# Kernel optimization log

Hardware: AMD Instinct MI355X
Metric: run time of the kernel (lower is better)

## Reference

```python
import jax, jax.numpy as jnp
import numpy as np

B, C, N, K = 2, 64, 16384, 16
C_OUT = 64


def setup_inputs() -> dict:
    key = jax.random.key(0)
    k1, k2, k3, k4 = jax.random.split(key, 4)
    x = jax.random.normal(k1, (B, C, N), dtype=jnp.float32)
    edge_index = jax.random.randint(k2, (2, B, N, K), 0, N, dtype=jnp.int64)
    # 1x1 Conv2d params: weight [C_out, 3C], bias [C_out]
    W = jax.random.normal(k3, (C_OUT, 3 * C), dtype=jnp.float32) * (1.0 / np.sqrt(3 * C))
    b = jax.random.normal(k4, (C_OUT,), dtype=jnp.float32) * 0.01
    return {"x": x, "edge_index": edge_index, "W": W, "b": b}


def _gather_nodes(x, idx):
    # x: [B, C, N], idx: [B, N, K] -> [B, C, N, K]
    return jax.vmap(lambda xb, ib: xb[:, ib])(x, idx)


def reference(x, edge_index, W, b):
    # x: [B, C, N]; edge_index: [2, B, N, K]
    x_i = _gather_nodes(x, edge_index[1])          # center features  [B,C,N,K]
    x_j = _gather_nodes(x, edge_index[0])          # neighbor features [B,C,N,K]
    edge_features = x_j - x_i                      # [B,C,N,K]
    global_feature = jnp.mean(x, axis=2, keepdims=True)  # [B,C,1] global mean over nodes
    global_rep = jnp.broadcast_to(global_feature[..., None], x_i.shape)  # [B,C,N,K]
    combined = jnp.concatenate([x_i, edge_features, global_rep], axis=1)  # [B,3C,N,K]
    # BasicConv: 1x1 conv + ReLU (norm=None)
    out = jnp.einsum("bcnk,oc->bonk", combined, W) + b[None, :, None, None]
    out = jax.nn.relu(out)
    return jnp.max(out, axis=-1, keepdims=True)    # [B,C_out,N,1]
```

## Files before the change

kernel.cpp:

```cpp
#include <hip/hip_runtime.h>


#define NNODES 16384
#define NCH 64

typedef _Float16 half8 __attribute__((ext_vector_type(8)));
typedef float f32x2 __attribute__((ext_vector_type(2)));
typedef float f32x4 __attribute__((ext_vector_type(4)));

__global__ __launch_bounds__(64) void prep_kernel(const float* __restrict__ W,
                                                  float2* __restrict__ ABg,
                                                  float* __restrict__ g_slots) {
  int o = blockIdx.x;
  int t = threadIdx.x;
  if (o == 0) {
#pragma unroll
    for (int i = 0; i < 16; ++i) g_slots[t + i * 64] = 0.0f;
  }
  float w1 = W[o * 192 + t];
  float w2 = W[o * 192 + 64 + t];
  ABg[t * 64 + o] = make_float2(w1 - w2, w2);
}

__global__ __launch_bounds__(256) void warmx_kernel(const float* __restrict__ x) {
  int t = threadIdx.x;
  int blk = blockIdx.x;
  int b = blk >> 8;
  int mb = (blk & 255) * 64;
  const float* xb = x + (size_t)b * (NCH * NNODES) + mb;
  int off = t & 15;
  float keep = 0.f;
#pragma unroll
  for (int j = 0; j < 4; ++j) {
    int c = (t >> 4) + j * 16;
    f32x4 q = *(const f32x4*)(xb + (size_t)c * NNODES + off * 4);
    keep += q.x;
  }
  asm volatile("" ::"v"(keep));
}

__global__ __launch_bounds__(256) void uv_kernel(const float* __restrict__ x,
                                                 const float2* __restrict__ ABg,
                                                 _Float16* __restrict__ u,
                                                 _Float16* __restrict__ v,
                                                 float* __restrict__ g_slots) {
  __shared__ float2 ABs[64 * 64];
  __shared__ float xs[64][64];
  __shared__ float csumS[64];
  int t = threadIdx.x;
  int lane = t & 63;
  int wv = __builtin_amdgcn_readfirstlane(t >> 6);
  int blk = blockIdx.x;
  int b = blk >> 8;
  int mb = (blk & 255) * 64;

  const float* xb = x + (size_t)b * (NCH * NNODES) + mb;
  int off = t & 15;
  f32x4 q0, q1, q2, q3;
  {
    q0 = __builtin_nontemporal_load((const f32x4*)(xb + (size_t)((t >> 4) + 0) * NNODES + off * 4));
    q1 = __builtin_nontemporal_load((const f32x4*)(xb + (size_t)((t >> 4) + 16) * NNODES + off * 4));
    q2 = __builtin_nontemporal_load((const f32x4*)(xb + (size_t)((t >> 4) + 32) * NNODES + off * 4));
    q3 = __builtin_nontemporal_load((const f32x4*)(xb + (size_t)((t >> 4) + 48) * NNODES + off * 4));
  }
  {
    const float4* src = (const float4*)ABg;
    float4* dst = (float4*)ABs;
#pragma unroll
    for (int j = 0; j < 8; ++j) dst[t + j * 256] = src[t + j * 256];
  }
  {
    f32x4 qq[4] = {q0, q1, q2, q3};
#pragma unroll
    for (int j = 0; j < 4; ++j) {
      int c = (t >> 4) + j * 16;
      *(f32x4*)&xs[c][off * 4] = qq[j];
      float s = (qq[j].x + qq[j].y) + (qq[j].z + qq[j].w);
      s += __shfl_xor(s, 1, 16);
      s += __shfl_xor(s, 2, 16);
      s += __shfl_xor(s, 4, 16);
      s += __shfl_xor(s, 8, 16);
      if (off == 0) csumS[c] = s;
    }
  }
  __syncthreads();
  if (t < 64) atomicAdd(&g_slots[((blk & 7) << 7) + b * 64 + t], csumS[t]);

  int m0 = wv * 16;
  f32x2 aU[8], aV[8];
#pragma unroll
  for (int i = 0; i < 8; ++i) {
    aU[i] = (f32x2){0.f, 0.f};
    aV[i] = (f32x2){0.f, 0.f};
  }
#pragma unroll 8
  for (int c = 0; c < 64; ++c) {
    float2 ab = ABs[c * 64 + lane];
    f32x2 a2 = {ab.x, ab.x};
    f32x2 b2 = {ab.y, ab.y};
    const f32x4* xr = (const f32x4*)&xs[c][m0];
    f32x4 p0q = xr[0];
    f32x4 p1q = xr[1];
    f32x4 p2q = xr[2];
    f32x4 p3q = xr[3];
    f32x2 p0 = {p0q.x, p0q.y}, p1 = {p0q.z, p0q.w};
    f32x2 p2 = {p1q.x, p1q.y}, p3 = {p1q.z, p1q.w};
    f32x2 p4 = {p2q.x, p2q.y}, p5 = {p2q.z, p2q.w};
    f32x2 p6 = {p3q.x, p3q.y}, p7 = {p3q.z, p3q.w};
    aU[0] = __builtin_elementwise_fma(a2, p0, aU[0]);
    aU[1] = __builtin_elementwise_fma(a2, p1, aU[1]);
    aU[2] = __builtin_elementwise_fma(a2, p2, aU[2]);
    aU[3] = __builtin_elementwise_fma(a2, p3, aU[3]);
    aU[4] = __builtin_elementwise_fma(a2, p4, aU[4]);
    aU[5] = __builtin_elementwise_fma(a2, p5, aU[5]);
    aU[6] = __builtin_elementwise_fma(a2, p6, aU[6]);
    aU[7] = __builtin_elementwise_fma(a2, p7, aU[7]);
    aV[0] = __builtin_elementwise_fma(b2, p0, aV[0]);
    aV[1] = __builtin_elementwise_fma(b2, p1, aV[1]);
    aV[2] = __builtin_elementwise_fma(b2, p2, aV[2]);
    aV[3] = __builtin_elementwise_fma(b2, p3, aV[3]);
    aV[4] = __builtin_elementwise_fma(b2, p4, aV[4]);
    aV[5] = __builtin_elementwise_fma(b2, p5, aV[5]);
    aV[6] = __builtin_elementwise_fma(b2, p6, aV[6]);
    aV[7] = __builtin_elementwise_fma(b2, p7, aV[7]);
  }
  _Float16* ub = u + ((size_t)b * NNODES + mb + m0) * NCH + lane;
  _Float16* vb = v + ((size_t)b * NNODES + mb + m0) * NCH + lane;
#pragma unroll
  for (int i = 0; i < 8; ++i) {
    __builtin_nontemporal_store((_Float16)aU[i][0], &ub[(2 * i) * NCH]);
    __builtin_nontemporal_store((_Float16)aU[i][1], &ub[(2 * i + 1) * NCH]);
    __builtin_nontemporal_store((_Float16)aV[i][0], &vb[(2 * i) * NCH]);
    __builtin_nontemporal_store((_Float16)aV[i][1], &vb[(2 * i + 1) * NCH]);
  }
}

__global__ __launch_bounds__(256) void gather_kernel(const int* __restrict__ ei,
                                                     const _Float16* __restrict__ u,
                                                     const _Float16* __restrict__ v,
                                                     const float* __restrict__ W,
                                                     const float* __restrict__ bias,
                                                     const float* __restrict__ g_slots,
                                                     float* __restrict__ out) {
  __shared__ float tile[64][33];
  __shared__ float gb[64];
  __shared__ float pg[4][64];
  __shared__ float G_s[64];
  int t = threadIdx.x;
  int lane = t & 63;
  int wv = t >> 6;
  int blk = blockIdx.x;
  int xcd = blk & 7;
  int b = xcd >> 2;
  int nb = (blk >> 3) * 4 + (xcd & 3);
  int n0 = nb * 32;
  int q = lane >> 3;
  int r = lane & 7;
  const int* e0b = ei + (size_t)b * NNODES * 16;
  const int* e1b = ei + (size_t)(2 + b) * NNODES * 16;
  int f0 = (n0 + wv * 8) * 16 + q * 16 + r;
  int i0a = __builtin_nontemporal_load(e0b + f0);
  int i0b = __builtin_nontemporal_load(e0b + f0 + 8);
  int i1a = __builtin_nontemporal_load(e1b + f0);
  int i1b = __builtin_nontemporal_load(e1b + f0 + 8);
  if (t < 64) {
    float s = 0.f;
#pragma unroll
    for (int sl = 0; sl < 8; ++sl) s += g_slots[sl * 128 + b * 64 + t];
    gb[t] = s * (1.0f / 16384.0f);
  }
  __syncthreads();
  {
    int o = t >> 2, cq = t & 3;
    const float4* wr = (const float4*)(W + o * 192 + 128 + cq * 16);
    const float4* gr = (const float4*)(gb + cq * 16);
    float s = 0.f;
#pragma unroll
    for (int j = 0; j < 4; ++j) {
      float4 w = wr[j];
      float4 gg = gr[j];
      s += w.x * gg.x + w.y * gg.y + w.z * gg.z + w.w * gg.w;
    }
    pg[cq][o] = s;
  }
  __syncthreads();
  if (t < 64) G_s[t] = bias[t] + ((pg[0][t] + pg[1][t]) + (pg[2][t] + pg[3][t]));
  __syncthreads();
  const char* ubase = (const char*)(u + (size_t)b * NNODES * NCH);
  const char* vbase = (const char*)(v + (size_t)b * NNODES * NCH);
  uint32_t r16 = (uint32_t)(r * 16);
  half8 accA, accB;
#pragma unroll
  for (int j = 0; j < 8; ++j) {
    accA[j] = (_Float16)(-60000.0f);
    accB[j] = (_Float16)(-60000.0f);
  }
#pragma unroll
  for (int h = 0; h < 2; ++h) {
    half8 ua[8], va[8];
#pragma unroll
    for (int k = 0; k < 8; ++k) {
      int src = (lane & 56) + k;
      int m1 = __shfl(h ? i1b : i1a, src, 64);
      int m0i = __shfl(h ? i0b : i0a, src, 64);
      ua[k] = *(const half8*)(ubase + ((uint32_t)m1 * 128u + r16));
      va[k] = *(const half8*)(vbase + ((uint32_t)m0i * 128u + r16));
    }
#pragma unroll
    for (int k = 0; k < 8; ++k) {
      half8 s = ua[k] + va[k];
      if (k & 1)
        accB = __builtin_elementwise_max(accB, s);
      else
        accA = __builtin_elementwise_max(accA, s);
    }
  }
  half8 acc = __builtin_elementwise_max(accA, accB);
  int col = wv * 8 + q;
#pragma unroll
  for (int j = 0; j < 8; ++j) {
    tile[r * 8 + j][col] = fmaxf((float)acc[j] + G_s[r * 8 + j], 0.0f);
  }
  __syncthreads();
#pragma unroll
  for (int j = 0; j < 8; ++j) {
    int o = (t >> 5) + j * 8;
    int c2 = t & 31;
    __builtin_nontemporal_store(tile[o][c2],
                                &out[((size_t)b * 64 + o) * NNODES + n0 + c2]);
  }
}

extern "C" void kernel_launch(void* const* d_in, const int* in_sizes, int n_in,
                              void* d_out, int out_size, void* d_ws, size_t ws_size,
                              hipStream_t stream) {
  const float* x = (const float*)d_in[0];
  const int* ei = (const int*)d_in[1];
  const float* W = (const float*)d_in[2];
  const float* bias = (const float*)d_in[3];
  float* out = (float*)d_out;

  char* ws = (char*)d_ws;
  _Float16* u = (_Float16*)ws;
  _Float16* v = (_Float16*)(ws + (size_t)4 * 1024 * 1024);
  float* g_slots = (float*)(ws + (size_t)8 * 1024 * 1024);
  float2* ABg = (float2*)(ws + (size_t)8 * 1024 * 1024 + 4096);

  prep_kernel<<<64, 64, 0, stream>>>(W, ABg, g_slots);
  warmx_kernel<<<512, 256, 0, stream>>>(x);
  uv_kernel<<<512, 256, 0, stream>>>(x, ABg, u, v, g_slots);
  gather_kernel<<<1024, 256, 0, stream>>>(ei, u, v, W, bias, g_slots, out);
}
```

Before: 90.83 us.

## Fold weight prep into uv kernel, prefetch edge indices, drop nontemporal loads

Removes the separate prep kernel: each uv block builds its shared weight table directly from W, and the global-sum slots are zeroed with hipMemsetAsync. The warm-up kernel now streams through both x and the edge-index array, and the later nontemporal loads become ordinary loads. The intent is to pull those inputs into cache before the main kernels read them and to cut one launch. In exchange, every uv block re-reads and transposes W with strided loads, and the warm pass adds extra memory traffic of its own.

```diff
diff --git a/kernel.cpp b/kernel.cpp
--- a/kernel.cpp
+++ b/kernel.cpp
@@ -8,39 +8,21 @@
 typedef float f32x2 __attribute__((ext_vector_type(2)));
 typedef float f32x4 __attribute__((ext_vector_type(4)));
 
-__global__ __launch_bounds__(64) void prep_kernel(const float* __restrict__ W,
-                                                  float2* __restrict__ ABg,
-                                                  float* __restrict__ g_slots) {
-  int o = blockIdx.x;
-  int t = threadIdx.x;
-  if (o == 0) {
-#pragma unroll
-    for (int i = 0; i < 16; ++i) g_slots[t + i * 64] = 0.0f;
-  }
-  float w1 = W[o * 192 + t];
-  float w2 = W[o * 192 + 64 + t];
-  ABg[t * 64 + o] = make_float2(w1 - w2, w2);
-}
-
-__global__ __launch_bounds__(256) void warmx_kernel(const float* __restrict__ x) {
+__global__ __launch_bounds__(256) void warm_kernel(const float* __restrict__ x,
+                                                   const int* __restrict__ ei) {
   int t = threadIdx.x;
   int blk = blockIdx.x;
-  int b = blk >> 8;
-  int mb = (blk & 255) * 64;
-  const float* xb = x + (size_t)b * (NCH * NNODES) + mb;
-  int off = t & 15;
-  float keep = 0.f;
-#pragma unroll
-  for (int j = 0; j < 4; ++j) {
-    int c = (t >> 4) + j * 16;
-    f32x4 q = *(const f32x4*)(xb + (size_t)c * NNODES + off * 4);
-    keep += q.x;
-  }
+  const f32x4* xp = (const f32x4*)x + (size_t)blk * 512 + t;
+  f32x4 a = xp[0];
+  f32x4 c = xp[256];
+  const f32x4* ep = (const f32x4*)ei + (size_t)blk * 256 + t;
+  f32x4 e = ep[0];
+  float keep = a.x + c.x + e.x;
   asm volatile("" ::"v"(keep));
 }
 
 __global__ __launch_bounds__(256) void uv_kernel(const float* __restrict__ x,
-                                                 const float2* __restrict__ ABg,
+                                                 const float* __restrict__ W,
                                                  _Float16* __restrict__ u,
                                                  _Float16* __restrict__ v,
                                                  float* __restrict__ g_slots) {
@@ -56,18 +38,19 @@
 
   const float* xb = x + (size_t)b * (NCH * NNODES) + mb;
   int off = t & 15;
-  f32x4 q0, q1, q2, q3;
+  f32x4 q0 = *(const f32x4*)(xb + (size_t)((t >> 4) + 0) * NNODES + off * 4);
+  f32x4 q1 = *(const f32x4*)(xb + (size_t)((t >> 4) + 16) * NNODES + off * 4);
+  f32x4 q2 = *(const f32x4*)(xb + (size_t)((t >> 4) + 32) * NNODES + off * 4);
+  f32x4 q3 = *(const f32x4*)(xb + (size_t)((t >> 4) + 48) * NNODES + off * 4);
   {
-    q0 = __builtin_nontemporal_load((const f32x4*)(xb + (size_t)((t >> 4) + 0) * NNODES + off * 4));
-    q1 = __builtin_nontemporal_load((const f32x4*)(xb + (size_t)((t >> 4) + 16) * NNODES + off * 4));
-    q2 = __builtin_nontemporal_load((const f32x4*)(xb + (size_t)((t >> 4) + 32) * NNODES + off * 4));
-    q3 = __builtin_nontemporal_load((const f32x4*)(xb + (size_t)((t >> 4) + 48) * NNODES + off * 4));
-  }
-  {
-    const float4* src = (const float4*)ABg;
-    float4* dst = (float4*)ABs;
-#pragma unroll
-    for (int j = 0; j < 8; ++j) dst[t + j * 256] = src[t + j * 256];
+    int o = t & 63, c0 = (t >> 6) * 16;
+    const float* wr = W + o * 192;
+#pragma unroll
+    for (int i = 0; i < 16; ++i) {
+      int c = c0 + i;
+      float w1 = wr[c], w2 = wr[64 + c];
+      ABs[c * 64 + o] = (float2){w1 - w2, w2};
+    }
   }
   {
     f32x4 qq[4] = {q0, q1, q2, q3};
@@ -159,10 +142,10 @@
   const int* e0b = ei + (size_t)b * NNODES * 16;
   const int* e1b = ei + (size_t)(2 + b) * NNODES * 16;
   int f0 = (n0 + wv * 8) * 16 + q * 16 + r;
-  int i0a = __builtin_nontemporal_load(e0b + f0);
-  int i0b = __builtin_nontemporal_load(e0b + f0 + 8);
-  int i1a = __builtin_nontemporal_load(e1b + f0);
-  int i1b = __builtin_nontemporal_load(e1b + f0 + 8);
+  int i0a = e0b[f0];
+  int i0b = e0b[f0 + 8];
+  int i1a = e1b[f0];
+  int i1b = e1b[f0 + 8];
   if (t < 64) {
     float s = 0.f;
 #pragma unroll
@@ -244,10 +227,9 @@
   _Float16* u = (_Float16*)ws;
   _Float16* v = (_Float16*)(ws + (size_t)4 * 1024 * 1024);
   float* g_slots = (float*)(ws + (size_t)8 * 1024 * 1024);
-  float2* ABg = (float2*)(ws + (size_t)8 * 1024 * 1024 + 4096);
-
-  prep_kernel<<<64, 64, 0, stream>>>(W, ABg, g_slots);
-  warmx_kernel<<<512, 256, 0, stream>>>(x);
-  uv_kernel<<<512, 256, 0, stream>>>(x, ABg, u, v, g_slots);
+
+  hipMemsetAsync(g_slots, 0, 8 * 128 * sizeof(float), stream);
+  warm_kernel<<<1024, 256, 0, stream>>>(x, ei);
+  uv_kernel<<<512, 256, 0, stream>>>(x, W, u, v, g_slots);
   gather_kernel<<<1024, 256, 0, stream>>>(ei, u, v, W, bias, g_slots, out);
 }
```

Result: slower. 92.96 us (+2.3%).
